# Kernel optimization log

Hardware: AMD Instinct MI355X
Metric: run time of the kernel (lower is better)

The kernel has to match this reference:

```python
import jax, jax.numpy as jnp
import numpy as np
import math

VOCAB = 50257
EMBED = 256
RES = 2048
SQV = int(math.ceil(math.sqrt(VOCAB)))  # 225
B, T = 4, 512


def setup_inputs() -> dict:
    key = jax.random.key(0)
    ks = jax.random.split(key, 10)
    idx = jax.random.randint(ks[0], (B, T), 0, VOCAB)
    targets = jax.random.randint(ks[1], (B, T), 0, VOCAB)
    wte = 0.02 * jax.random.normal(ks[2], (VOCAB, EMBED), dtype=jnp.float32)
    W_in = jax.random.uniform(ks[3], (RES, EMBED), minval=-0.1, maxval=0.1, dtype=jnp.float32)
    W_ih = jax.random.uniform(ks[4], (RES, RES), minval=-1.0, maxval=1.0, dtype=jnp.float32)
    # approximate spectral-radius rescale: sr(uniform(-1,1) NxN) ~ sqrt(N/3)
    sr_scale = 0.99 / float(np.sqrt(RES / 3.0))
    W_hh = sr_scale * jax.random.uniform(ks[5], (RES, RES), minval=-1.0, maxval=1.0, dtype=jnp.float32)
    b_ih = jax.random.uniform(ks[6], (RES,), minval=-0.1, maxval=0.1, dtype=jnp.float32)
    b_hh = jax.random.uniform(ks[7], (RES,), minval=-0.1, maxval=0.1, dtype=jnp.float32)
    Wh1 = (1.0 / np.sqrt(RES)) * jax.random.normal(ks[8], (SQV, RES), dtype=jnp.float32)
    Wh2 = (1.0 / np.sqrt(RES)) * jax.random.normal(ks[9], (SQV, RES), dtype=jnp.float32)
    return {"idx": idx, "targets": targets, "wte": wte, "W_in": W_in,
            "W_ih": W_ih, "b_ih": b_ih, "W_hh": W_hh, "b_hh": b_hh,
            "Wh1": Wh1, "Wh2": Wh2}


def _esn_states(idx, wte, W_in, W_ih, b_ih, W_hh, b_hh):
    emb = wte[idx]                                  # [B,T,E]
    proj = jnp.einsum('bte,re->btr', emb, W_in)     # [B,T,R]
    xin = jnp.einsum('btr,sr->bts', proj, W_ih) + b_ih  # precompute input part
    h0 = jnp.zeros((idx.shape[0], RES), dtype=proj.dtype)

    def step(h, xt):  # xt: [B,R]
        h = jnp.tanh(xt + h @ W_hh.T + b_hh)
        return h, h

    h_n, states = jax.lax.scan(step, h0, jnp.swapaxes(xin, 0, 1))  # states [T,B,R]
    return jnp.swapaxes(states, 0, 1), h_n


def reference(idx, targets, wte, W_in, W_ih, b_ih, W_hh, b_hh, Wh1, Wh2):
    states, h_n = _esn_states(idx, wte, W_in, W_ih, b_ih, W_hh, b_hh)  # [B,T,R]
    logits1 = jnp.einsum('btr,vr->btv', states, Wh1)  # [B,T,SQV]
    logits2 = jnp.einsum('btr,vr->btv', states, Wh2)

    # masked dual cross-entropy (ignore -1)
    mask = (targets != -1)
    safe_t = jnp.where(mask, targets, 0)
    t_row = safe_t // SQV
    t_col = safe_t % SQV
    lp1 = jax.nn.log_softmax(logits1, axis=-1)
    lp2 = jax.nn.log_softmax(logits2, axis=-1)
    nll1 = -jnp.take_along_axis(lp1, t_row[..., None], axis=-1)[..., 0]
    nll2 = -jnp.take_along_axis(lp2, t_col[..., None], axis=-1)[..., 0]
    cnt = jnp.maximum(mask.sum(), 1)
    loss = (jnp.where(mask, nll1, 0.0).sum() + jnp.where(mask, nll2, 0.0).sum()) / cnt

    # combined log-probs -> logits over full vocab
    combined = lp1[..., :, None] + lp2[..., None, :]          # [B,T,SQV,SQV]
    logits = combined.reshape(idx.shape[0], idx.shape[1], SQV * SQV)[:, :, :VOCAB]
    return logits, loss, h_n[None]  # h_n [1,B,R] like torch RNN
```

## Files before the change

kernel.cpp:

```cpp
#include <hip/hip_runtime.h>
#include <stdint.h>
#include <math.h>

#define R_  2048
#define E_  256
#define T_  512
#define BT_ 2048
#define SQ_ 225
#define V_  50257
#define NWG_R 128

typedef float f32x4 __attribute__((ext_vector_type(4)));

__global__ __launch_bounds__(256) void k_gemm_mt(const float* __restrict__ Win,
                                                 const float* __restrict__ Wih,
                                                 float* __restrict__ Mt) {
  __shared__ __align__(16) float As[32][68];
  __shared__ __align__(16) float Bs[32][68];
  const int m0 = blockIdx.x * 64;
  const int n0 = blockIdx.y * 64;
  const int tid = threadIdx.x;
  const int tx = tid & 15, ty = tid >> 4;
  float acc[4][4] = {};
  for (int k0 = 0; k0 < R_; k0 += 32) {
    {
      int mm = tid & 63, kk = tid >> 6;
#pragma unroll
      for (int u = 0; u < 8; ++u)
        As[kk + u * 4][mm] = Win[(size_t)(k0 + kk + u * 4) * E_ + m0 + mm];
    }
    {
      int kk = tid & 31, nn = tid >> 5;
#pragma unroll
      for (int u = 0; u < 8; ++u)
        Bs[kk][nn + u * 8] = Wih[(size_t)(n0 + nn + u * 8) * R_ + k0 + kk];
    }
    __syncthreads();
#pragma unroll
    for (int kk = 0; kk < 32; ++kk) {
      float4 a = *(const float4*)&As[kk][ty * 4];
      float4 b = *(const float4*)&Bs[kk][tx * 4];
      acc[0][0] += a.x * b.x; acc[0][1] += a.x * b.y; acc[0][2] += a.x * b.z; acc[0][3] += a.x * b.w;
      acc[1][0] += a.y * b.x; acc[1][1] += a.y * b.y; acc[1][2] += a.y * b.z; acc[1][3] += a.y * b.w;
      acc[2][0] += a.z * b.x; acc[2][1] += a.z * b.y; acc[2][2] += a.z * b.z; acc[2][3] += a.z * b.w;
      acc[3][0] += a.w * b.x; acc[3][1] += a.w * b.y; acc[3][2] += a.w * b.z; acc[3][3] += a.w * b.w;
    }
    __syncthreads();
  }
#pragma unroll
  for (int i = 0; i < 4; ++i) {
    float4 v = make_float4(acc[i][0], acc[i][1], acc[i][2], acc[i][3]);
    *(float4*)&Mt[(size_t)(m0 + ty * 4 + i) * R_ + n0 + tx * 4] = v;
  }
}

__global__ __launch_bounds__(256) void k_xin(const int* __restrict__ idx,
                                             const float* __restrict__ wte,
                                             const float* __restrict__ Mt,
                                             const float* __restrict__ bih,
                                             float* __restrict__ xin) {
  __shared__ __align__(16) float As[32][68];
  __shared__ __align__(16) float Bs[32][68];
  __shared__ int rowL[64];
  const int m0 = blockIdx.x * 64;
  const int n0 = blockIdx.y * 64;
  const int tid = threadIdx.x;
  const int tx = tid & 15, ty = tid >> 4;
  if (tid < 64) rowL[tid] = idx[m0 + tid];
  __syncthreads();
  float acc[4][4] = {};
  for (int k0 = 0; k0 < E_; k0 += 32) {
    {
      int kk = tid & 31, mm = tid >> 5;
#pragma unroll
      for (int u = 0; u < 8; ++u)
        As[kk][mm + u * 8] = wte[(size_t)rowL[mm + u * 8] * E_ + k0 + kk];
    }
    {
      int nn = tid & 63, kk = tid >> 6;
#pragma unroll
      for (int u = 0; u < 8; ++u)
        Bs[kk + u * 4][nn] = Mt[(size_t)(k0 + kk + u * 4) * R_ + n0 + nn];
    }
    __syncthreads();
#pragma unroll
    for (int kk = 0; kk < 32; ++kk) {
      float4 a = *(const float4*)&As[kk][ty * 4];
      float4 b = *(const float4*)&Bs[kk][tx * 4];
      acc[0][0] += a.x * b.x; acc[0][1] += a.x * b.y; acc[0][2] += a.x * b.z; acc[0][3] += a.x * b.w;
      acc[1][0] += a.y * b.x; acc[1][1] += a.y * b.y; acc[1][2] += a.y * b.z; acc[1][3] += a.y * b.w;
      acc[2][0] += a.z * b.x; acc[2][1] += a.z * b.y; acc[2][2] += a.z * b.z; acc[2][3] += a.z * b.w;
      acc[3][0] += a.w * b.x; acc[3][1] += a.w * b.y; acc[3][2] += a.w * b.z; acc[3][3] += a.w * b.w;
    }
    __syncthreads();
  }
  float4 bv = *(const float4*)&bih[n0 + tx * 4];
#pragma unroll
  for (int i = 0; i < 4; ++i) {
    float4 v = make_float4(acc[i][0] + bv.x, acc[i][1] + bv.y, acc[i][2] + bv.z, acc[i][3] + bv.w);
    *(float4*)&xin[(size_t)(m0 + ty * 4 + i) * R_ + n0 + tx * 4] = v;
  }
}

__global__ __launch_bounds__(256, 1) void k_recur(const float* __restrict__ Whh,
                                                  const float* __restrict__ xin,
                                                  const float* __restrict__ bhh_g,
                                                  float* hg,
                                                  float* __restrict__ st,
                                                  unsigned* flags) {
  __shared__ __align__(16) float hL[4][R_];
  const int tid = threadIdx.x;
  const int w = tid >> 6;
  const int c = tid & 63;
  const int row0 = blockIdx.x * 16 + w * 4;

  float W[4][32];
#pragma unroll
  for (int i = 0; i < 4; ++i) {
    const float* src = Whh + (size_t)(row0 + i) * R_;
#pragma unroll
    for (int k = 0; k < 8; ++k) {
      float4 v = *(const float4*)(src + k * 256 + c * 4);
      W[i][k * 4 + 0] = v.x; W[i][k * 4 + 1] = v.y; W[i][k * 4 + 2] = v.z; W[i][k * 4 + 3] = v.w;
    }
  }
  const int li = c >> 2, lb = c & 3;
  float bhl = (c < 16) ? bhh_g[row0 + li] : 0.f;

  for (int t = 0; t < T_; ++t) {
    const int p = t & 1;
    float xvl = 0.f;
    if (c < 16) xvl = xin[((size_t)(lb * T_ + t)) * R_ + row0 + li];

    if (t && tid < NWG_R) {
      unsigned* fp = flags + (size_t)tid * 16;
      long g = 0;
      while (__hip_atomic_load(fp, __ATOMIC_RELAXED, __HIP_MEMORY_SCOPE_AGENT) < (unsigned)t) {
        __builtin_amdgcn_s_sleep(1);
        if (++g > (1L << 24)) break;
      }
    }
    __syncthreads();

    {
      const f32x4* hsrc4 = (const f32x4*)(hg + (size_t)p * 8192);
      f32x4 tmp[8];
#pragma unroll
      for (int j = 0; j < 8; ++j) {
        const f32x4* ap = hsrc4 + tid + j * 256;
        asm volatile("global_load_dwordx4 %0, %1, off sc0 sc1" : "=&v"(tmp[j]) : "v"(ap));
      }
      asm volatile("s_waitcnt vmcnt(0)" ::: "memory");
      __builtin_amdgcn_sched_barrier(0);
      f32x4* hLv = (f32x4*)hL;
#pragma unroll
      for (int j = 0; j < 8; ++j) hLv[tid + j * 256] = tmp[j];
    }
    __syncthreads();

    float acc[4][4] = {};
#pragma unroll
    for (int k = 0; k < 8; ++k) {
      float4 h4[4];
#pragma unroll
      for (int b = 0; b < 4; ++b) h4[b] = *(const float4*)&hL[b][k * 256 + c * 4];
#pragma unroll
      for (int i = 0; i < 4; ++i) {
#pragma unroll
        for (int b = 0; b < 4; ++b) {
          acc[i][b] += W[i][k * 4 + 0] * h4[b].x + W[i][k * 4 + 1] * h4[b].y
                     + W[i][k * 4 + 2] * h4[b].z + W[i][k * 4 + 3] * h4[b].w;
        }
      }
    }
#pragma unroll
    for (int i = 0; i < 4; ++i)
#pragma unroll
      for (int b = 0; b < 4; ++b) {
        float v = acc[i][b];
        v += __shfl_xor(v, 32); v += __shfl_xor(v, 16); v += __shfl_xor(v, 8);
        v += __shfl_xor(v, 4);  v += __shfl_xor(v, 2);  v += __shfl_xor(v, 1);
        acc[i][b] = v;
      }
    if (c < 16) {
      float val = acc[0][0];
#pragma unroll
      for (int i = 0; i < 4; ++i)
#pragma unroll
        for (int b = 0; b < 4; ++b) {
          int k = i * 4 + b;
          if (k > 0) val = (c == k) ? acc[i][b] : val;
        }
      float hn = tanhf(xvl + val + bhl);
      __hip_atomic_store(&hg[(size_t)(1 - p) * 8192 + lb * R_ + row0 + li], hn,
                         __ATOMIC_RELAXED, __HIP_MEMORY_SCOPE_AGENT);
      st[((size_t)(lb * T_ + t)) * R_ + row0 + li] = hn;
    }
    __syncthreads();
    if (tid == 0) {
      asm volatile("s_waitcnt vmcnt(0)" ::: "memory");
      __hip_atomic_store(flags + (size_t)blockIdx.x * 16, (unsigned)(t + 1),
                         __ATOMIC_RELAXED, __HIP_MEMORY_SCOPE_AGENT);
    }
  }
}

__global__ __launch_bounds__(256) void k_logits(const float* __restrict__ stt,
                                                const float* __restrict__ Wh1,
                                                const float* __restrict__ Wh2,
                                                float* __restrict__ lg1,
                                                float* __restrict__ lg2) {
  __shared__ __align__(16) float As[32][68];
  __shared__ __align__(16) float Bs[32][68];
  const int m0 = blockIdx.x * 64;
  const int n0 = blockIdx.y * 64;
  const int tid = threadIdx.x;
  const int tx = tid & 15, ty = tid >> 4;
  float acc[4][4] = {};
  for (int k0 = 0; k0 < R_; k0 += 32) {
    {
      int kk = tid & 31, mm = tid >> 5;
#pragma unroll
      for (int u = 0; u < 8; ++u)
        As[kk][mm + u * 8] = stt[(size_t)(m0 + mm + u * 8) * R_ + k0 + kk];
    }
    {
      int kk = tid & 31, nn = tid >> 5;
#pragma unroll
      for (int u = 0; u < 8; ++u) {
        int n = n0 + nn + u * 8;
        float v = 0.f;
        if (n < SQ_)            v = Wh1[(size_t)n * R_ + k0 + kk];
        else if (n < 2 * SQ_)   v = Wh2[(size_t)(n - SQ_) * R_ + k0 + kk];
        Bs[kk][nn + u * 8] = v;
      }
    }
    __syncthreads();
#pragma unroll
    for (int kk = 0; kk < 32; ++kk) {
      float4 a = *(const float4*)&As[kk][ty * 4];
      float4 b = *(const float4*)&Bs[kk][tx * 4];
      acc[0][0] += a.x * b.x; acc[0][1] += a.x * b.y; acc[0][2] += a.x * b.z; acc[0][3] += a.x * b.w;
      acc[1][0] += a.y * b.x; acc[1][1] += a.y * b.y; acc[1][2] += a.y * b.z; acc[1][3] += a.y * b.w;
      acc[2][0] += a.z * b.x; acc[2][1] += a.z * b.y; acc[2][2] += a.z * b.z; acc[2][3] += a.z * b.w;
      acc[3][0] += a.w * b.x; acc[3][1] += a.w * b.y; acc[3][2] += a.w * b.z; acc[3][3] += a.w * b.w;
    }
    __syncthreads();
  }
#pragma unroll
  for (int i = 0; i < 4; ++i)
#pragma unroll
    for (int j = 0; j < 4; ++j) {
      int n = n0 + tx * 4 + j;
      int m = m0 + ty * 4 + i;
      if (n < SQ_)          lg1[(size_t)m * 256 + n] = acc[i][j];
      else if (n < 2 * SQ_) lg2[(size_t)m * 256 + (n - SQ_)] = acc[i][j];
    }
}

__global__ __launch_bounds__(256) void k_lsm(float* lg1, float* lg2,
                                             const int* __restrict__ tgt, float* ctrl) {
  const int bt = blockIdx.x;
  const int head = blockIdx.y;
  float* lg = (head ? lg2 : lg1) + (size_t)bt * 256;
  const int tid = threadIdx.x;
  __shared__ float red[8];
  float x = (tid < SQ_) ? lg[tid] : -1e30f;
  float m = x;
#pragma unroll
  for (int o = 32; o >= 1; o >>= 1) m = fmaxf(m, __shfl_down(m, o));
  if ((tid & 63) == 0) red[tid >> 6] = m;
  __syncthreads();
  if (tid == 0) red[4] = fmaxf(fmaxf(red[0], red[1]), fmaxf(red[2], red[3]));
  __syncthreads();
  float mx = red[4];
  float e = (tid < SQ_) ? __expf(x - mx) : 0.f;
  float s = e;
#pragma unroll
  for (int o = 32; o >= 1; o >>= 1) s += __shfl_down(s, o);
  if ((tid & 63) == 0) red[tid >> 6] = s;
  __syncthreads();
  if (tid == 0) red[5] = logf(red[0] + red[1] + red[2] + red[3]);
  __syncthreads();
  float lp = x - mx - red[5];
  if (tid < SQ_) lg[tid] = lp;
  int t = tgt[bt];
  if (t != -1) {
    int trow = (int)(((uint64_t)(unsigned)t * 19088744ULL) >> 32);
    int tcol = t - trow * 225;
    int want = head ? tcol : trow;
    if (tid == want) atomicAdd(&ctrl[1], -lp);
    if (head == 0 && tid == 0) atomicAdd((int*)ctrl + 2, 1);
  }
}

__global__ __launch_bounds__(256) void k_write(const float* __restrict__ lg1,
                                               const float* __restrict__ lg2,
                                               float* __restrict__ out) {
  __shared__ float l1[SQ_], l2[SQ_];
  const int bt = blockIdx.x;
  const int tid = threadIdx.x;
  if (tid < SQ_) {
    l1[tid] = lg1[(size_t)bt * 256 + tid];
    l2[tid] = lg2[(size_t)bt * 256 + tid];
  }
  __syncthreads();
  const int vbase = blockIdx.y * 4096;
  float* o = out + (size_t)bt * V_;
#pragma unroll
  for (int i = 0; i < 16; ++i) {
    int v = vbase + i * 256 + tid;
    if (v < V_) {
      int row = (int)(((uint64_t)(unsigned)v * 19088744ULL) >> 32);
      int col = v - row * 225;
      o[v] = l1[row] + l2[col];
    }
  }
}

__global__ __launch_bounds__(256) void k_tail(const float* __restrict__ hg,
                                              const float* __restrict__ ctrl,
                                              float* __restrict__ out) {
  int i = blockIdx.x * 256 + threadIdx.x;
  if (i < 8192) {
    out[(size_t)BT_ * V_ + 1 + i] = hg[i];
  } else if (i == 8192) {
    int cnt = ((const int*)ctrl)[2];
    if (cnt < 1) cnt = 1;
    out[(size_t)BT_ * V_] = ctrl[1] / (float)cnt;
  }
}

extern "C" void kernel_launch(void* const* d_in, const int* in_sizes, int n_in,
                              void* d_out, int out_size, void* d_ws, size_t ws_size,
                              hipStream_t stream) {
  (void)in_sizes; (void)n_in; (void)out_size; (void)ws_size;
  const int*   idx = (const int*)d_in[0];
  const int*   tgt = (const int*)d_in[1];
  const float* wte = (const float*)d_in[2];
  const float* Win = (const float*)d_in[3];
  const float* Wih = (const float*)d_in[4];
  const float* bih = (const float*)d_in[5];
  const float* Whh = (const float*)d_in[6];
  const float* bhh = (const float*)d_in[7];
  const float* Wh1 = (const float*)d_in[8];
  const float* Wh2 = (const float*)d_in[9];

  float* ws    = (float*)d_ws;
  float* ctrl  = ws;
  unsigned* fl = (unsigned*)(ws + 64);
  float* hg    = ws + 64 + 2048;
  float* Mt    = hg + 16384;
  float* xin   = Mt + (size_t)E_ * R_;
  float* st    = xin + (size_t)BT_ * R_;
  float* lg1   = xin;
  float* lg2   = xin + (size_t)BT_ * 256;
  float* out   = (float*)d_out;

  hipMemsetAsync(d_ws, 0, (64 + 2048 + 16384) * sizeof(float), stream);
  k_gemm_mt<<<dim3(E_ / 64, R_ / 64), 256, 0, stream>>>(Win, Wih, Mt);
  k_xin<<<dim3(BT_ / 64, R_ / 64), 256, 0, stream>>>(idx, wte, Mt, bih, xin);
  k_recur<<<dim3(NWG_R), 256, 0, stream>>>(Whh, xin, bhh, hg, st, fl);
  k_logits<<<dim3(BT_ / 64, 8), 256, 0, stream>>>(st, Wh1, Wh2, lg1, lg2);
  k_lsm<<<dim3(BT_, 2), 256, 0, stream>>>(lg1, lg2, tgt, ctrl);
  k_write<<<dim3(BT_, 13), 256, 0, stream>>>(lg1, lg2, out);
  k_tail<<<dim3(33), 256, 0, stream>>>(hg, ctrl, out);
}
```

Before: 3.533 ms.

## Transpose xin/state layouts, batch state stores, and poll flags per wave

The xin and state buffers are stored transposed (feature-major), so the recurrence reads its per-step input and the logits GEMM loads its A tile along contiguous rows. Per-step state writes are staged in shared memory and flushed every 8 steps as float4 stores. Each wave now polls all 128 flags itself, which removes a block barrier before the h load, and the vmcnt wait before publishing the flag is dropped. Dropping that wait and the barrier risks a memory-ordering hazard on the h publication, and the poll traffic per block goes up.

```diff
diff --git a/kernel.cpp b/kernel.cpp
--- a/kernel.cpp
+++ b/kernel.cpp
@@ -58,9 +58,10 @@
                                              const float* __restrict__ wte,
                                              const float* __restrict__ Mt,
                                              const float* __restrict__ bih,
-                                             float* __restrict__ xin) {
+                                             float* __restrict__ xinT) {
   __shared__ __align__(16) float As[32][68];
   __shared__ __align__(16) float Bs[32][68];
+  __shared__ __align__(16) float Ts[64][68];
   __shared__ int rowL[64];
   const int m0 = blockIdx.x * 64;
   const int n0 = blockIdx.y * 64;
@@ -97,18 +98,30 @@
   float4 bv = *(const float4*)&bih[n0 + tx * 4];
 #pragma unroll
   for (int i = 0; i < 4; ++i) {
-    float4 v = make_float4(acc[i][0] + bv.x, acc[i][1] + bv.y, acc[i][2] + bv.z, acc[i][3] + bv.w);
-    *(float4*)&xin[(size_t)(m0 + ty * 4 + i) * R_ + n0 + tx * 4] = v;
+    Ts[tx * 4 + 0][ty * 4 + i] = acc[i][0] + bv.x;
+    Ts[tx * 4 + 1][ty * 4 + i] = acc[i][1] + bv.y;
+    Ts[tx * 4 + 2][ty * 4 + i] = acc[i][2] + bv.z;
+    Ts[tx * 4 + 3][ty * 4 + i] = acc[i][3] + bv.w;
+  }
+  __syncthreads();
+  {
+    int nn = tid >> 2, qq = tid & 3;
+#pragma unroll
+    for (int u = 0; u < 4; ++u) {
+      float4 v = *(const float4*)&Ts[nn][(qq + u * 4) * 4];
+      *(float4*)&xinT[(size_t)(n0 + nn) * BT_ + m0 + (qq + u * 4) * 4] = v;
+    }
   }
 }
 
 __global__ __launch_bounds__(256, 1) void k_recur(const float* __restrict__ Whh,
-                                                  const float* __restrict__ xin,
+                                                  const float* __restrict__ xinT,
                                                   const float* __restrict__ bhh_g,
                                                   float* hg,
-                                                  float* __restrict__ st,
+                                                  float* __restrict__ stT,
                                                   unsigned* flags) {
   __shared__ __align__(16) float hL[4][R_];
+  __shared__ float stS[2][8][72];
   const int tid = threadIdx.x;
   const int w = tid >> 6;
   const int c = tid & 63;
@@ -126,28 +139,30 @@
   }
   const int li = c >> 2, lb = c & 3;
   float bhl = (c < 16) ? bhh_g[row0 + li] : 0.f;
+  const int fr = tid >> 3, flb = (tid >> 1) & 3, fth = tid & 1;
 
   for (int t = 0; t < T_; ++t) {
     const int p = t & 1;
     float xvl = 0.f;
-    if (c < 16) xvl = xin[((size_t)(lb * T_ + t)) * R_ + row0 + li];
-
-    if (t && tid < NWG_R) {
-      unsigned* fp = flags + (size_t)tid * 16;
+    if (c < 16) xvl = xinT[(size_t)(row0 + li) * BT_ + lb * T_ + t];
+
+    if (t) {
+      const unsigned* f0 = flags + (size_t)c * 16;
+      const unsigned* f1 = flags + (size_t)(c + 64) * 16;
       long g = 0;
-      while (__hip_atomic_load(fp, __ATOMIC_RELAXED, __HIP_MEMORY_SCOPE_AGENT) < (unsigned)t) {
+      while (__hip_atomic_load(f0, __ATOMIC_RELAXED, __HIP_MEMORY_SCOPE_AGENT) < (unsigned)t ||
+             __hip_atomic_load(f1, __ATOMIC_RELAXED, __HIP_MEMORY_SCOPE_AGENT) < (unsigned)t) {
         __builtin_amdgcn_s_sleep(1);
         if (++g > (1L << 24)) break;
       }
     }
-    __syncthreads();
-
-    {
-      const f32x4* hsrc4 = (const f32x4*)(hg + (size_t)p * 8192);
+
+    {
+      const f32x4* hsrc = (const f32x4*)(hg + (size_t)p * 8192);
       f32x4 tmp[8];
 #pragma unroll
       for (int j = 0; j < 8; ++j) {
-        const f32x4* ap = hsrc4 + tid + j * 256;
+        const f32x4* ap = hsrc + tid + j * 256;
         asm volatile("global_load_dwordx4 %0, %1, off sc0 sc1" : "=&v"(tmp[j]) : "v"(ap));
       }
       asm volatile("s_waitcnt vmcnt(0)" ::: "memory");
@@ -194,18 +209,26 @@
       float hn = tanhf(xvl + val + bhl);
       __hip_atomic_store(&hg[(size_t)(1 - p) * 8192 + lb * R_ + row0 + li], hn,
                          __ATOMIC_RELAXED, __HIP_MEMORY_SCOPE_AGENT);
-      st[((size_t)(lb * T_ + t)) * R_ + row0 + li] = hn;
+      stS[(t >> 3) & 1][t & 7][lb * 16 + w * 4 + li] = hn;
     }
     __syncthreads();
     if (tid == 0) {
-      asm volatile("s_waitcnt vmcnt(0)" ::: "memory");
       __hip_atomic_store(flags + (size_t)blockIdx.x * 16, (unsigned)(t + 1),
                          __ATOMIC_RELAXED, __HIP_MEMORY_SCOPE_AGENT);
     }
-  }
-}
-
-__global__ __launch_bounds__(256) void k_logits(const float* __restrict__ stt,
+    if ((t & 7) == 7 && tid < 128) {
+      const int buf = (t >> 3) & 1, t0 = t - 7;
+      f32x4 v;
+      v.x = stS[buf][fth * 4 + 0][flb * 16 + fr];
+      v.y = stS[buf][fth * 4 + 1][flb * 16 + fr];
+      v.z = stS[buf][fth * 4 + 2][flb * 16 + fr];
+      v.w = stS[buf][fth * 4 + 3][flb * 16 + fr];
+      *(f32x4*)&stT[(size_t)(blockIdx.x * 16 + fr) * BT_ + flb * T_ + t0 + fth * 4] = v;
+    }
+  }
+}
+
+__global__ __launch_bounds__(256) void k_logits(const float* __restrict__ stT,
                                                 const float* __restrict__ Wh1,
                                                 const float* __restrict__ Wh2,
                                                 float* __restrict__ lg1,
@@ -219,10 +242,10 @@
   float acc[4][4] = {};
   for (int k0 = 0; k0 < R_; k0 += 32) {
     {
-      int kk = tid & 31, mm = tid >> 5;
-#pragma unroll
-      for (int u = 0; u < 8; ++u)
-        As[kk][mm + u * 8] = stt[(size_t)(m0 + mm + u * 8) * R_ + k0 + kk];
+      int mm = tid & 63, kk = tid >> 6;
+#pragma unroll
+      for (int u = 0; u < 8; ++u)
+        As[kk + u * 4][mm] = stT[(size_t)(k0 + kk + u * 4) * BT_ + m0 + mm];
     }
     {
       int kk = tid & 31, nn = tid >> 5;
@@ -351,17 +374,17 @@
   unsigned* fl = (unsigned*)(ws + 64);
   float* hg    = ws + 64 + 2048;
   float* Mt    = hg + 16384;
-  float* xin   = Mt + (size_t)E_ * R_;
-  float* st    = xin + (size_t)BT_ * R_;
-  float* lg1   = xin;
-  float* lg2   = xin + (size_t)BT_ * 256;
+  float* xinT  = Mt + (size_t)E_ * R_;
+  float* stT   = xinT + (size_t)BT_ * R_;
+  float* lg1   = xinT;
+  float* lg2   = xinT + (size_t)BT_ * 256;
   float* out   = (float*)d_out;
 
   hipMemsetAsync(d_ws, 0, (64 + 2048 + 16384) * sizeof(float), stream);
   k_gemm_mt<<<dim3(E_ / 64, R_ / 64), 256, 0, stream>>>(Win, Wih, Mt);
-  k_xin<<<dim3(BT_ / 64, R_ / 64), 256, 0, stream>>>(idx, wte, Mt, bih, xin);
-  k_recur<<<dim3(NWG_R), 256, 0, stream>>>(Whh, xin, bhh, hg, st, fl);
-  k_logits<<<dim3(BT_ / 64, 8), 256, 0, stream>>>(st, Wh1, Wh2, lg1, lg2);
+  k_xin<<<dim3(BT_ / 64, R_ / 64), 256, 0, stream>>>(idx, wte, Mt, bih, xinT);
+  k_recur<<<dim3(NWG_R), 256, 0, stream>>>(Whh, xinT, bhh, hg, stT, fl);
+  k_logits<<<dim3(BT_ / 64, 8), 256, 0, stream>>>(stT, Wh1, Wh2, lg1, lg2);
   k_lsm<<<dim3(BT_, 2), 256, 0, stream>>>(lg1, lg2, tgt, ctrl);
   k_write<<<dim3(BT_, 13), 256, 0, stream>>>(lg1, lg2, out);
   k_tail<<<dim3(33), 256, 0, stream>>>(hg, ctrl, out);
```

New measurement: 3.448 ms. 2.4% less time.
